# Kernel optimization log

Measured on AMD Instinct MI355X. Metric: run time of the kernel, lower is better.

## Reference

```python
import jax, jax.numpy as jnp
import numpy as np

FLOW_ITERS = 8
DUAL_ITERS = 8
DUAL_STEP = 0.1
DUAL_MOM = 0.9
GRAPH_LAYERS = 2
BIG = 1e9


def _sparsemax(z, mask):
    # sparsemax along last axis; masked entries already hold -BIG, zeroed by mask after.
    V = z.shape[-1]
    zs = jnp.sort(z, axis=-1)[..., ::-1]
    cum = jnp.cumsum(zs, axis=-1)
    k = jnp.arange(1, V + 1, dtype=z.dtype)
    support = zs * k > (cum - 1.0)
    k_sel = jnp.sum(support.astype(jnp.int32), axis=-1, keepdims=True)
    tau = (jnp.take_along_axis(cum, k_sel - 1, axis=-1) - 1.0) / k_sel.astype(z.dtype)
    return jnp.maximum(z - tau, 0.0) * mask


def _min_cost_flow(props, demands):
    # iterative proportional flow routing: push relu(inflow - demand) along predicted proportions
    def body(flow, _):
        inflow = jnp.sum(flow, axis=1)[..., None]      # [B,V,1] inflow to each node
        adjusted = jax.nn.relu(inflow - demands)       # excess to re-route
        return props * adjusted, None                  # row i scaled by its excess
    flow0 = jnp.zeros_like(props)
    flow, _ = jax.lax.scan(body, flow0, None, length=FLOW_ITERS)
    return flow


def _dual_flow(dual_diff, adj):
    # Nesterov-momentum projected gradient on cost(x)=x^2 minus linear dual term, x>=0 on edges
    def body(carry, _):
        flow, acc = carry
        look = flow - DUAL_MOM * acc
        grad = 2.0 * look - dual_diff                  # d/dx x^2 - dual_diff
        acc = DUAL_MOM * acc + DUAL_STEP * grad
        flow = adj * jax.nn.relu(flow - acc)
        return (flow, acc), None
    z = jnp.zeros_like(dual_diff)
    (flow, _), _ = jax.lax.scan(body, (z, z), None, length=DUAL_ITERS)
    return flow


def setup_inputs():
    key = jax.random.key(0)
    ks = jax.random.split(key, 32)
    B, V, F, E, D, K, H = 8, 1200, 8, 16, 64, 2, 4
    node_features = jax.random.normal(ks[0], (B, V, F), dtype=jnp.float32)
    node_embeddings = jax.random.normal(ks[1], (B, V, E), dtype=jnp.float32)
    d = jax.random.normal(ks[2], (B, V, 1), dtype=jnp.float32)
    demands = d - jnp.mean(d, axis=1, keepdims=True)   # balanced supply/demand per graph
    eye = jnp.eye(V, dtype=jnp.float32)
    adj = (jax.random.uniform(ks[3], (B, V, V)) < (16.0 / V)).astype(jnp.float32) * (1.0 - eye)
    hop2 = jnp.clip(adj @ adj, 0.0, 1.0) * (1.0 - eye)
    neighborhoods = jnp.stack([adj, hop2], axis=0)     # [K,B,V,V] k-hop neighborhoods

    def dense(k, fin, fout):
        return (jax.random.normal(k, (fin, fout), dtype=jnp.float32) / np.sqrt(fin)).astype(jnp.float32)

    return dict(
        node_features=node_features, node_embeddings=node_embeddings,
        demands=demands, adj=adj, neighborhoods=neighborhoods,
        enc_w0=dense(ks[4], E + F, D), enc_b0=jnp.zeros((D,), jnp.float32),
        enc_w1=dense(ks[5], D, D), enc_b1=jnp.zeros((D,), jnp.float32),
        agg_w=(jax.random.normal(ks[6], (K, D, D)) / np.sqrt(D)).astype(jnp.float32),
        agg_b=jnp.zeros((K, D), jnp.float32),
        att_w=(jax.random.normal(ks[7], (H, D, D)) / np.sqrt(D)).astype(jnp.float32),
        att_b=jnp.zeros((H, D), jnp.float32),
        att_v=(jax.random.normal(ks[8], (H, D)) / np.sqrt(D)).astype(jnp.float32),
        gru_wu=dense(ks[9], 2 * D, D), gru_bu=jnp.zeros((D,), jnp.float32),
        gru_wr=dense(ks[10], 2 * D, D), gru_br=jnp.zeros((D,), jnp.float32),
        gru_wc=dense(ks[11], 2 * D, D), gru_bc=jnp.zeros((D,), jnp.float32),
        dec_w0=dense(ks[12], D, D), dec_b0=jnp.zeros((D,), jnp.float32),
        dec_w1=dense(ks[13], D, 1), dec_b1=jnp.zeros((1,), jnp.float32),
        dual_w0=dense(ks[14], D, D), dual_b0=jnp.zeros((D,), jnp.float32),
        dual_w1=dense(ks[15], D, 1), dual_b1=jnp.zeros((1,), jnp.float32),
    )


def reference(node_features, node_embeddings, demands, adj, neighborhoods,
              enc_w0, enc_b0, enc_w1, enc_b1, agg_w, agg_b, att_w, att_b, att_v,
              gru_wu, gru_bu, gru_wr, gru_br, gru_wc, gru_bc,
              dec_w0, dec_b0, dec_w1, dec_b1, dual_w0, dual_b0, dual_w1, dual_b1):
    H = att_w.shape[0]
    # node encoder MLP (tanh hidden, tanh final since activate_final=True)
    x = jnp.concatenate([node_embeddings, node_features], axis=-1)
    enc = jnp.tanh(jnp.tanh(x @ enc_w0 + enc_b0) @ enc_w1 + enc_b1)            # [B,V,D]

    deg = jnp.sum(neighborhoods, axis=-1, keepdims=True)
    nb_norm = neighborhoods / jnp.maximum(deg, 1.0)                            # [K,B,V,V]

    for _ in range(GRAPH_LAYERS):
        # per-hop neighborhood aggregation
        msg = jnp.einsum('kbuv,bvd->kbud', nb_norm, enc)
        agg = jnp.tanh(jnp.einsum('kbud,kde->kbue', msg, agg_w) + agg_b[:, None, None, :])
        # multi-head attention over the K hop levels
        proj = jnp.tanh(jnp.einsum('kbvd,hde->hkbve', agg, att_w) + att_b[:, None, None, None, :])
        scores = jnp.einsum('hkbve,he->hkbv', proj, att_v)
        attn = jax.nn.softmax(scores, axis=1)                                  # softmax over hops
        nxt = jnp.einsum('hkbv,kbvd->bvd', attn, agg) / H                      # mean over heads
        # GRU state update
        xs = jnp.concatenate([nxt, enc], axis=-1)
        u = jax.nn.sigmoid(xs @ gru_wu + gru_bu)
        r = jax.nn.sigmoid(xs @ gru_wr + gru_br)
        c = jnp.tanh(jnp.concatenate([nxt, r * enc], axis=-1) @ gru_wc + gru_bc)
        enc = u * enc + (1.0 - u) * c

    # primal: edge weights -> sparsemax -> min-cost-flow
    pred = (enc @ dec_w0 + dec_b0) @ dec_w1 + dec_b1                           # [B,V,1]
    pred_weights = adj * jnp.transpose(pred, (0, 2, 1))                        # [B,V,V]
    weights = -BIG * (1.0 - adj) + pred_weights
    flow_props = _sparsemax(weights, adj)
    flow = _min_cost_flow(flow_props, demands)
    flow_cost = jnp.sum(flow * flow, axis=(1, 2))                              # square cost

    # dual: potentials -> dual-diff -> dual flow solver
    dual = (enc @ dual_w0 + dual_b0) @ dual_w1 + dual_b1                       # [B,V,1]
    dual_diff = adj * (dual - jnp.transpose(dual, (0, 2, 1)))
    dflow = _dual_flow(dual_diff, adj)
    dual_demand = jnp.sum(dual * demands, axis=(1, 2))
    dual_cost = jnp.sum(dflow * dflow - dual_diff * dflow, axis=(1, 2)) - dual_demand

    return flow_cost - dual_cost                                               # duality-gap loss, [B]
```

## Files before the change

### kernel.cpp

```cpp
#include <hip/hip_runtime.h>

#define BB 8
#define VV 1200
#define DD 64
#define KH 2
#define NH 4
#define CAP 64
#define NB2CAP 384
#define NROW (BB*VV)
#define NKROW (KH*BB*VV)

__device__ __forceinline__ float wredsum(float v) {
#pragma unroll
  for (int o = 32; o > 0; o >>= 1) v += __shfl_xor(v, o, 64);
  return v;
}
__device__ __forceinline__ float gredsum32(float v) {
#pragma unroll
  for (int o = 16; o > 0; o >>= 1) v += __shfl_xor(v, o, 64);
  return v;
}

__device__ __forceinline__ float tanh_f(float x) {
  float e = __expf(2.0f * x);
  return 1.0f - 2.0f / (e + 1.0f);
}
__device__ __forceinline__ float sigmoid_f(float x) { return 1.0f / (1.0f + __expf(-x)); }

__device__ __forceinline__ size_t nb_base(int row) {
  return (row < NROW) ? (size_t)row * CAP
                      : (size_t)NROW * CAP + (size_t)(row - NROW) * NB2CAP;
}

#define ENC2B (NROW / 64)
#define CSR2B (NKROW / 8)
__global__ void __launch_bounds__(512) k_pre(
    const float* __restrict__ nb, int* __restrict__ nb_cols, int* __restrict__ nb_cnt,
    const float* __restrict__ emb, const float* __restrict__ feat,
    const float* __restrict__ w0, const float* __restrict__ b0,
    const float* __restrict__ w1, const float* __restrict__ b1,
    float* __restrict__ enc0,
    int* __restrict__ col_cnt, float* __restrict__ out, int out_size) {
  __shared__ float Xe[64][25];
  __shared__ float Ht[64][65];
  __shared__ int colS[8][NB2CAP];
  int bid = blockIdx.x;
  int tid = threadIdx.x;
  if (bid < ENC2B) {
    int tile0 = bid * 64;
    if (tid < 256) {
      int i = tid >> 2, f = tid & 3;
      float4 e4 = *(const float4*)(emb + (size_t)(tile0 + i) * 16 + f * 4);
      Xe[i][f * 4] = e4.x; Xe[i][f * 4 + 1] = e4.y; Xe[i][f * 4 + 2] = e4.z; Xe[i][f * 4 + 3] = e4.w;
    } else if (tid < 384) {
      int t = tid - 256; int i = t >> 1, f = t & 1;
      float4 f4 = *(const float4*)(feat + (size_t)(tile0 + i) * 8 + f * 4);
      Xe[i][16 + f * 4] = f4.x; Xe[i][16 + f * 4 + 1] = f4.y;
      Xe[i][16 + f * 4 + 2] = f4.z; Xe[i][16 + f * 4 + 3] = f4.w;
    }
    __syncthreads();
    int rsub = tid >> 4, cg = tid & 15;
    int c0 = cg * 4, r0 = rsub * 2;
    float a[2][4];
#pragma unroll
    for (int i = 0; i < 2; ++i)
#pragma unroll
      for (int j = 0; j < 4; ++j) a[i][j] = b0[c0 + j];
#pragma unroll
    for (int kk = 0; kk < 24; ++kk) {
      float4 w4 = *(const float4*)(w0 + kk * DD + c0);
      float x0 = Xe[r0][kk], x1 = Xe[r0 + 1][kk];
      a[0][0] = fmaf(x0, w4.x, a[0][0]); a[0][1] = fmaf(x0, w4.y, a[0][1]);
      a[0][2] = fmaf(x0, w4.z, a[0][2]); a[0][3] = fmaf(x0, w4.w, a[0][3]);
      a[1][0] = fmaf(x1, w4.x, a[1][0]); a[1][1] = fmaf(x1, w4.y, a[1][1]);
      a[1][2] = fmaf(x1, w4.z, a[1][2]); a[1][3] = fmaf(x1, w4.w, a[1][3]);
    }
#pragma unroll
    for (int i = 0; i < 2; ++i) {
      Ht[r0 + i][c0] = tanh_f(a[i][0]); Ht[r0 + i][c0 + 1] = tanh_f(a[i][1]);
      Ht[r0 + i][c0 + 2] = tanh_f(a[i][2]); Ht[r0 + i][c0 + 3] = tanh_f(a[i][3]);
    }
    __syncthreads();
    float g[2][4];
#pragma unroll
    for (int i = 0; i < 2; ++i)
#pragma unroll
      for (int j = 0; j < 4; ++j) g[i][j] = b1[c0 + j];
#pragma unroll 8
    for (int kk = 0; kk < DD; ++kk) {
      float4 w4 = *(const float4*)(w1 + kk * DD + c0);
      float x0 = Ht[r0][kk], x1 = Ht[r0 + 1][kk];
      g[0][0] = fmaf(x0, w4.x, g[0][0]); g[0][1] = fmaf(x0, w4.y, g[0][1]);
      g[0][2] = fmaf(x0, w4.z, g[0][2]); g[0][3] = fmaf(x0, w4.w, g[0][3]);
      g[1][0] = fmaf(x1, w4.x, g[1][0]); g[1][1] = fmaf(x1, w4.y, g[1][1]);
      g[1][2] = fmaf(x1, w4.z, g[1][2]); g[1][3] = fmaf(x1, w4.w, g[1][3]);
    }
#pragma unroll
    for (int i = 0; i < 2; ++i) {
      float4 o;
      o.x = tanh_f(g[i][0]); o.y = tanh_f(g[i][1]);
      o.z = tanh_f(g[i][2]); o.w = tanh_f(g[i][3]);
      *(float4*)(enc0 + (size_t)(tile0 + r0 + i) * DD + c0) = o;
    }
  } else if (bid < ENC2B + CSR2B) {
    int w = tid >> 6, lane = tid & 63;
    int row = (bid - ENC2B) * 8 + w;
    const float4* nb4 = (const float4*)(nb + (size_t)row * VV);
    float4 v[5];
#pragma unroll
    for (int c = 0; c < 4; ++c) v[c] = nb4[c * 64 + lane];
    v[4].x = v[4].y = v[4].z = v[4].w = 0.0f;
    if (lane < 44) v[4] = nb4[256 + lane];
    unsigned long long ltmask = (lane == 0) ? 0ull : ((1ull << lane) - 1ull);
    size_t base = nb_base(row);
    int cap = (row < NROW) ? CAP : NB2CAP;
    int off_base = 0;
#pragma unroll
    for (int c = 0; c < 5; ++c) {
      int nz0 = (v[c].x != 0.0f), nz1 = (v[c].y != 0.0f);
      int nz2 = (v[c].z != 0.0f), nz3 = (v[c].w != 0.0f);
      unsigned long long m0 = __ballot(nz0 != 0);
      unsigned long long m1 = __ballot(nz1 != 0);
      unsigned long long m2 = __ballot(nz2 != 0);
      unsigned long long m3 = __ballot(nz3 != 0);
      int lanepref = __popcll(m0 & ltmask) + __popcll(m1 & ltmask)
                   + __popcll(m2 & ltmask) + __popcll(m3 & ltmask);
      int chunkcnt = __popcll(m0) + __popcll(m1) + __popcll(m2) + __popcll(m3);
      int off = off_base + lanepref;
      int vi = (c * 64 + lane) * 4;
      if (nz0 && off < cap) colS[w][off] = vi;
      off += nz0;
      if (nz1 && off < cap) colS[w][off] = vi + 1;
      off += nz1;
      if (nz2 && off < cap) colS[w][off] = vi + 2;
      off += nz2;
      if (nz3 && off < cap) colS[w][off] = vi + 3;
      off_base += chunkcnt;
    }
    int ncp = (off_base > cap) ? cap : off_base;
    if (lane == 0) nb_cnt[row] = ncp;
    for (int j = lane; j < ncp; j += 64) nb_cols[base + j] = colS[w][j];
  } else {
    for (int i = tid; i < NROW; i += 512) col_cnt[i] = 0;
    if (tid < out_size) out[tid] = 0.0f;
  }
}

__global__ void __launch_bounds__(256) k_gather(
    const int* __restrict__ nb_cols, const int* __restrict__ nb_cnt,
    const float* __restrict__ encIn, float* __restrict__ msg) {
  int w = threadIdx.x >> 6, lane = threadIdx.x & 63;
  int row = blockIdx.x * 4 + w;
  int k = (row >= NROW) ? 1 : 0;
  int bv = row - k * NROW;
  int b = bv / VV;
  const float4* encF = (const float4*)(encIn + (size_t)b * VV * DD);
  const int* cols = nb_cols + nb_base(row);
  int n = nb_cnt[row];
  int sub = lane >> 4, q = lane & 15;
  float ax = 0.0f, ay = 0.0f, az = 0.0f, aw = 0.0f;
  int j = 0;
  int cc0 = 0, cc1 = 0, cc2 = 0, cc3 = 0;
  if (j + 16 <= n) {
    cc0 = cols[j + sub]; cc1 = cols[j + 4 + sub];
    cc2 = cols[j + 8 + sub]; cc3 = cols[j + 12 + sub];
  }
  while (j + 16 <= n) {
    int nj = j + 16;
    int p0 = 0, p1 = 0, p2 = 0, p3 = 0;
    if (nj + 16 <= n) {
      p0 = cols[nj + sub]; p1 = cols[nj + 4 + sub];
      p2 = cols[nj + 8 + sub]; p3 = cols[nj + 12 + sub];
    }
    float4 u0 = encF[(size_t)cc0 * 16 + q];
    float4 u1 = encF[(size_t)cc1 * 16 + q];
    float4 u2 = encF[(size_t)cc2 * 16 + q];
    float4 u3 = encF[(size_t)cc3 * 16 + q];
    ax += (u0.x + u1.x) + (u2.x + u3.x);
    ay += (u0.y + u1.y) + (u2.y + u3.y);
    az += (u0.z + u1.z) + (u2.z + u3.z);
    aw += (u0.w + u1.w) + (u2.w + u3.w);
    cc0 = p0; cc1 = p1; cc2 = p2; cc3 = p3;
    j = nj;
  }
  for (; j < n; j += 4) {
    int idx = j + sub;
    if (idx < n) {
      float4 u = encF[(size_t)cols[idx] * 16 + q];
      ax += u.x; ay += u.y; az += u.z; aw += u.w;
    }
  }
#pragma unroll
  for (int o = 16; o < 64; o <<= 1) {
    ax += __shfl_xor(ax, o, 64);
    ay += __shfl_xor(ay, o, 64);
    az += __shfl_xor(az, o, 64);
    aw += __shfl_xor(aw, o, 64);
  }
  if (lane < 16) {
    float inv = 1.0f / fmaxf((float)n, 1.0f);
    float4 r; r.x = ax * inv; r.y = ay * inv; r.z = az * inv; r.w = aw * inv;
    ((float4*)(msg + (size_t)row * DD))[q] = r;
  }
}

__global__ void __launch_bounds__(256) k_layer(
    const float* __restrict__ msg, const float* __restrict__ encIn,
    const float* __restrict__ agg_w, const float* __restrict__ agg_b,
    const float* __restrict__ att_w, const float* __restrict__ att_b,
    const float* __restrict__ att_v,
    const float* __restrict__ wu, const float* __restrict__ bu,
    const float* __restrict__ wr, const float* __restrict__ br,
    const float* __restrict__ wc, const float* __restrict__ bc,
    float* __restrict__ encOut,
    int do_decode,
    const float* __restrict__ dw0, const float* __restrict__ db0,
    const float* __restrict__ dw1, const float* __restrict__ db1,
    const float* __restrict__ uw0, const float* __restrict__ ub0,
    const float* __restrict__ uw1, const float* __restrict__ ub1,
    float* __restrict__ pred, float* __restrict__ dualp) {
  __shared__ float M[32][65];
  __shared__ float G[32][65];
  __shared__ float X[16][129];
  __shared__ float EO[16][65];
  __shared__ float scS[NH][KH][16];
  int tid = threadIdx.x;
  int t0 = blockIdx.x * 16;
#pragma unroll
  for (int rep = 0; rep < 2; ++rep) {
    int idx = rep * 256 + tid; int i = idx >> 4, d4 = idx & 15;
    int grow = (i < 16) ? (t0 + i) : (NROW + t0 + (i - 16));
    float4 m4 = *(const float4*)(msg + (size_t)grow * DD + d4 * 4);
    M[i][d4 * 4] = m4.x; M[i][d4 * 4 + 1] = m4.y; M[i][d4 * 4 + 2] = m4.z; M[i][d4 * 4 + 3] = m4.w;
  }
  __syncthreads();
  int strip = tid >> 5, cg2 = tid & 31;
  int c0 = cg2 * 2;
  int r0 = strip * 4;
  int k = strip >> 2;
  const float* W = agg_w + (size_t)k * DD * DD;
  float acc[4][2];
#pragma unroll
  for (int i = 0; i < 4; ++i) {
    acc[i][0] = agg_b[k * DD + c0]; acc[i][1] = agg_b[k * DD + c0 + 1];
  }
#pragma unroll 8
  for (int kk = 0; kk < DD; ++kk) {
    float2 w2 = *(const float2*)(W + kk * DD + c0);
#pragma unroll
    for (int i = 0; i < 4; ++i) {
      float x = M[r0 + i][kk];
      acc[i][0] = fmaf(x, w2.x, acc[i][0]); acc[i][1] = fmaf(x, w2.y, acc[i][1]);
    }
  }
#pragma unroll
  for (int i = 0; i < 4; ++i) {
    G[r0 + i][c0] = tanh_f(acc[i][0]);
    G[r0 + i][c0 + 1] = tanh_f(acc[i][1]);
  }
  __syncthreads();
#pragma unroll
  for (int h = 0; h < NH; ++h) {
    const float* Wh = att_w + (size_t)h * DD * DD;
    float a2[4][2];
#pragma unroll
    for (int i = 0; i < 4; ++i) {
      a2[i][0] = att_b[h * DD + c0]; a2[i][1] = att_b[h * DD + c0 + 1];
    }
#pragma unroll 8
    for (int kk = 0; kk < DD; ++kk) {
      float2 w2 = *(const float2*)(Wh + kk * DD + c0);
#pragma unroll
      for (int i = 0; i < 4; ++i) {
        float x = G[r0 + i][kk];
        a2[i][0] = fmaf(x, w2.x, a2[i][0]); a2[i][1] = fmaf(x, w2.y, a2[i][1]);
      }
    }
    float2 v2 = *(const float2*)(att_v + h * DD + c0);
#pragma unroll
    for (int i = 0; i < 4; ++i) {
      float p = tanh_f(a2[i][0]) * v2.x + tanh_f(a2[i][1]) * v2.y;
      p = gredsum32(p);
      if (cg2 == 0) scS[h][k][(strip & 3) * 4 + i] = p;
    }
  }
  __syncthreads();
  {
    int i = tid >> 4, d4 = tid & 15;
    float W0 = 0.0f, W1 = 0.0f;
#pragma unroll
    for (int h = 0; h < NH; ++h) {
      float s0 = scS[h][0][i];
      float s1 = scS[h][1][i];
      float m = fmaxf(s0, s1);
      float e0 = __expf(s0 - m), e1 = __expf(s1 - m);
      float inv = 1.0f / (e0 + e1);
      W0 += e0 * inv; W1 += e1 * inv;
    }
    W0 *= 0.25f; W1 *= 0.25f;
    float4 ef = *(const float4*)(encIn + (size_t)(t0 + i) * DD + d4 * 4);
#pragma unroll
    for (int j = 0; j < 4; ++j) {
      int d = d4 * 4 + j;
      X[i][d] = W0 * G[i][d] + W1 * G[16 + i][d];
    }
    X[i][64 + d4 * 4]     = ef.x;
    X[i][64 + d4 * 4 + 1] = ef.y;
    X[i][64 + d4 * 4 + 2] = ef.z;
    X[i][64 + d4 * 4 + 3] = ef.w;
  }
  __syncthreads();
  int gr0 = strip * 2;
  float au[2][2], ar[2][2];
#pragma unroll
  for (int i = 0; i < 2; ++i) {
    au[i][0] = bu[c0]; au[i][1] = bu[c0 + 1];
    ar[i][0] = br[c0]; ar[i][1] = br[c0 + 1];
  }
#pragma unroll 8
  for (int kk = 0; kk < 2 * DD; ++kk) {
    float2 u2 = *(const float2*)(wu + kk * DD + c0);
    float2 r2 = *(const float2*)(wr + kk * DD + c0);
#pragma unroll
    for (int i = 0; i < 2; ++i) {
      float x = X[gr0 + i][kk];
      au[i][0] = fmaf(x, u2.x, au[i][0]); au[i][1] = fmaf(x, u2.y, au[i][1]);
      ar[i][0] = fmaf(x, r2.x, ar[i][0]); ar[i][1] = fmaf(x, r2.y, ar[i][1]);
    }
  }
  float uu[2][2], encv[2][2];
#pragma unroll
  for (int i = 0; i < 2; ++i) {
    uu[i][0] = sigmoid_f(au[i][0]); uu[i][1] = sigmoid_f(au[i][1]);
    encv[i][0] = X[gr0 + i][64 + c0]; encv[i][1] = X[gr0 + i][64 + c0 + 1];
  }
  __syncthreads();
#pragma unroll
  for (int i = 0; i < 2; ++i) {
    X[gr0 + i][64 + c0]     = encv[i][0] * sigmoid_f(ar[i][0]);
    X[gr0 + i][64 + c0 + 1] = encv[i][1] * sigmoid_f(ar[i][1]);
  }
  __syncthreads();
  float ac[2][2];
#pragma unroll
  for (int i = 0; i < 2; ++i) { ac[i][0] = bc[c0]; ac[i][1] = bc[c0 + 1]; }
#pragma unroll 8
  for (int kk = 0; kk < 2 * DD; ++kk) {
    float2 c2 = *(const float2*)(wc + kk * DD + c0);
#pragma unroll
    for (int i = 0; i < 2; ++i) {
      float x = X[gr0 + i][kk];
      ac[i][0] = fmaf(x, c2.x, ac[i][0]); ac[i][1] = fmaf(x, c2.y, ac[i][1]);
    }
  }
#pragma unroll
  for (int i = 0; i < 2; ++i) {
    float e0 = uu[i][0] * encv[i][0] + (1.0f - uu[i][0]) * tanh_f(ac[i][0]);
    float e1 = uu[i][1] * encv[i][1] + (1.0f - uu[i][1]) * tanh_f(ac[i][1]);
    *(float2*)(encOut + (size_t)(t0 + gr0 + i) * DD + c0) = make_float2(e0, e1);
    EO[gr0 + i][c0] = e0; EO[gr0 + i][c0 + 1] = e1;
  }
  if (do_decode) {
    __syncthreads();
    float hd[2][2], hq[2][2];
#pragma unroll
    for (int i = 0; i < 2; ++i) {
      hd[i][0] = db0[c0]; hd[i][1] = db0[c0 + 1];
      hq[i][0] = ub0[c0]; hq[i][1] = ub0[c0 + 1];
    }
#pragma unroll 8
    for (int kk = 0; kk < DD; ++kk) {
      float2 d2 = *(const float2*)(dw0 + kk * DD + c0);
      float2 q2 = *(const float2*)(uw0 + kk * DD + c0);
#pragma unroll
      for (int i = 0; i < 2; ++i) {
        float x = EO[gr0 + i][kk];
        hd[i][0] = fmaf(x, d2.x, hd[i][0]); hd[i][1] = fmaf(x, d2.y, hd[i][1]);
        hq[i][0] = fmaf(x, q2.x, hq[i][0]); hq[i][1] = fmaf(x, q2.y, hq[i][1]);
      }
    }
    float2 dv = *(const float2*)(dw1 + c0);
    float2 qv = *(const float2*)(uw1 + c0);
#pragma unroll
    for (int i = 0; i < 2; ++i) {
      float p = hd[i][0] * dv.x + hd[i][1] * dv.y;
      float q = hq[i][0] * qv.x + hq[i][1] * qv.y;
      p = gredsum32(p);
      q = gredsum32(q);
      if (cg2 == 0) {
        pred[t0 + gr0 + i] = p + db1[0];
        dualp[t0 + gr0 + i] = q + ub1[0];
      }
    }
  }
}

__global__ void __launch_bounds__(256) k_primal_dual(
    const int* __restrict__ nb_cols, const int* __restrict__ nb_cnt,
    const float* __restrict__ pred, const float* __restrict__ dualp,
    const float* __restrict__ dem,
    float* __restrict__ rowsum,
    int* __restrict__ col_cnt, int* __restrict__ col_rows, float* __restrict__ col_vals,
    float* __restrict__ out) {
  __shared__ float bacc[BB];
  if (threadIdx.x < BB) bacc[threadIdx.x] = 0.0f;
  __syncthreads();
  int w = threadIdx.x >> 6, lane = threadIdx.x & 63;
  int row = blockIdx.x * 4 + w;
  int b = row / VV;
  int n = nb_cnt[row];
  int c = (lane < n) ? nb_cols[(size_t)row * CAP + lane] : 0;
  const float* predB = pred + (size_t)b * VV;
  const float* dualB = dualp + (size_t)b * VV;
  float z = (lane < n) ? predB[c] : -1e30f;
  float tau = 0.0f;
  if (n > 0) {
    bool in = (lane < n);
    for (int it = 0; it < 64; ++it) {
      float s = wredsum(in ? z : 0.0f);
      int cnt = (int)__popcll(__ballot(in));
      tau = (s - 1.0f) / (float)cnt;
      bool nin = (z > tau);
      if (__ballot(nin) == __ballot(in)) break;
      in = nin;
    }
  }
  float pv = (lane < n) ? fmaxf(z - tau, 0.0f) : 0.0f;
  float s2 = wredsum(pv * pv);
  if (lane == 0) rowsum[row] = s2;
  if (pv > 0.0f) {
    int g = b * VV + c;
    int j = atomicAdd(&col_cnt[g], 1);
    if (j < CAP) {
      col_rows[(size_t)g * CAP + j] = row - b * VV;
      col_vals[(size_t)g * CAP + j] = pv;
    }
  }
  float du = dualp[row];
  float es = 0.0f;
  if (lane < n) {
    float dd = du - dualB[c];
    float f = 0.0f, acm = 0.0f;
#pragma unroll
    for (int t = 0; t < 8; ++t) {
      float look = f - 0.9f * acm;
      float grad = 2.0f * look - dd;
      acm = 0.9f * acm + 0.1f * grad;
      f = fmaxf(f - acm, 0.0f);
    }
    es = f * f - dd * f;
  }
  float contrib = -es;
  if (lane == 0) contrib += du * dem[row];
  float ws_ = wredsum(contrib);
  if (lane == 0) atomicAdd(&bacc[b], ws_);
  __syncthreads();
  if (threadIdx.x < BB) {
    float t = bacc[threadIdx.x];
    if (t != 0.0f) atomicAdd(&out[threadIdx.x], t);
  }
}

__global__ void __launch_bounds__(1024) k_flow(
    const int* __restrict__ col_cnt, const int* __restrict__ col_rows,
    const float* __restrict__ col_vals, const float* __restrict__ dem,
    const float* __restrict__ rowsum, float* __restrict__ out) {
  __shared__ float aS[VV];
  __shared__ float red[16];
  int b = blockIdx.x;
  int tid = threadIdx.x;
  const float* demB = dem + (size_t)b * VV;
  for (int v = tid; v < VV; v += 1024) aS[v] = fmaxf(-demB[v], 0.0f);
  __syncthreads();
  for (int t = 0; t < 7; ++t) {
    float nv0 = 0.0f, nv1 = 0.0f;
    {
      int v = tid;
      if (v < VV) {
        int g = b * VV + v;
        int n = col_cnt[g]; if (n > CAP) n = CAP;
        const int* cr = col_rows + (size_t)g * CAP;
        const float* cv = col_vals + (size_t)g * CAP;
        float acc = 0.0f;
        for (int j = 0; j < n; ++j) acc += cv[j] * aS[cr[j]];
        nv0 = fmaxf(acc - demB[v], 0.0f);
      }
      v = tid + 1024;
      if (v < VV) {
        int g = b * VV + v;
        int n = col_cnt[g]; if (n > CAP) n = CAP;
        const int* cr = col_rows + (size_t)g * CAP;
        const float* cv = col_vals + (size_t)g * CAP;
        float acc = 0.0f;
        for (int j = 0; j < n; ++j) acc += cv[j] * aS[cr[j]];
        nv1 = fmaxf(acc - demB[v], 0.0f);
      }
    }
    __syncthreads();
    if (tid < VV) aS[tid] = nv0;
    if (tid + 1024 < VV) aS[tid + 1024] = nv1;
    __syncthreads();
  }
  float fc = 0.0f;
  for (int v = tid; v < VV; v += 1024) { float a = aS[v]; fc += a * a * rowsum[b * VV + v]; }
  fc = wredsum(fc);
  int wid = tid >> 6, lane = tid & 63;
  if (lane == 0) red[wid] = fc;
  __syncthreads();
  if (tid == 0) {
    float s = 0.0f;
#pragma unroll
    for (int i = 0; i < 16; ++i) s += red[i];
    atomicAdd(&out[b], s);
  }
}

extern "C" void kernel_launch(void* const* d_in, const int* in_sizes, int n_in,
                              void* d_out, int out_size, void* d_ws, size_t ws_size,
                              hipStream_t stream) {
  const float* feat   = (const float*)d_in[0];
  const float* emb    = (const float*)d_in[1];
  const float* dem    = (const float*)d_in[2];
  const float* nb     = (const float*)d_in[4];
  const float* enc_w0 = (const float*)d_in[5];
  const float* enc_b0 = (const float*)d_in[6];
  const float* enc_w1 = (const float*)d_in[7];
  const float* enc_b1 = (const float*)d_in[8];
  const float* agg_w  = (const float*)d_in[9];
  const float* agg_b  = (const float*)d_in[10];
  const float* att_w  = (const float*)d_in[11];
  const float* att_b  = (const float*)d_in[12];
  const float* att_v  = (const float*)d_in[13];
  const float* gru_wu = (const float*)d_in[14];
  const float* gru_bu = (const float*)d_in[15];
  const float* gru_wr = (const float*)d_in[16];
  const float* gru_br = (const float*)d_in[17];
  const float* gru_wc = (const float*)d_in[18];
  const float* gru_bc = (const float*)d_in[19];
  const float* dec_w0 = (const float*)d_in[20];
  const float* dec_b0 = (const float*)d_in[21];
  const float* dec_w1 = (const float*)d_in[22];
  const float* dec_b1 = (const float*)d_in[23];
  const float* dual_w0= (const float*)d_in[24];
  const float* dual_b0= (const float*)d_in[25];
  const float* dual_w1= (const float*)d_in[26];
  const float* dual_b1= (const float*)d_in[27];
  float* out = (float*)d_out;

  float* enc0 = (float*)d_ws;
  float* enc1 = enc0 + (size_t)NROW * DD;
  float* msg      = enc1 + (size_t)NROW * DD;
  float* pred     = msg + (size_t)NKROW * DD;
  float* dualp    = pred + NROW;
  float* rowsum   = dualp + NROW;
  float* col_vals = rowsum + NROW;
  int* col_cnt  = (int*)(col_vals + (size_t)NROW * CAP);
  int* nb_cnt   = col_cnt + NROW;
  int* col_rows = nb_cnt + NKROW;
  int* nb_cols  = col_rows + (size_t)NROW * CAP;

  (void)in_sizes; (void)n_in; (void)ws_size;

  k_pre<<<ENC2B + CSR2B + 1, 512, 0, stream>>>(
      nb, nb_cols, nb_cnt, emb, feat, enc_w0, enc_b0, enc_w1, enc_b1, enc0,
      col_cnt, out, out_size);

  const float* encIn = enc0;
  float* encOut = enc1;
  for (int l = 0; l < 2; ++l) {
    k_gather<<<NKROW / 4, 256, 0, stream>>>(nb_cols, nb_cnt, encIn, msg);
    k_layer<<<NROW / 16, 256, 0, stream>>>(msg, encIn,
                                           agg_w, agg_b, att_w, att_b, att_v,
                                           gru_wu, gru_bu, gru_wr, gru_br, gru_wc, gru_bc,
                                           encOut,
                                           (l == 1) ? 1 : 0,
                                           dec_w0, dec_b0, dec_w1, dec_b1,
                                           dual_w0, dual_b0, dual_w1, dual_b1, pred, dualp);
    const float* t = encIn; encIn = encOut; encOut = (float*)t;
  }

  k_primal_dual<<<NROW / 4, 256, 0, stream>>>(nb_cols, nb_cnt, pred, dualp, dem,
                                              rowsum, col_cnt, col_rows, col_vals, out);
  k_flow<<<BB, 1024, 0, stream>>>(col_cnt, col_rows, col_vals, dem, rowsum, out);
}
```

Before: 514.4 us.

## Stage layer weight matrices through shared memory instead of global loads

The k_layer kernel now cooperatively copies each weight matrix (agg, attention in two halves, GRU u/r/c, decoder) into a 32KB shared buffer before the matching matmul, and reads weights from LDS instead of global/L2 per-thread float2 loads. To fit, M and G are merged into one buffer, and the fused u/r GEMV is split into two passes. This trades repeated global weight traffic per block for extra syncthreads, large staging copies per block (600 blocks each reloading all weights), and higher LDS use that may cut occupancy.

```diff
diff --git a/kernel.cpp b/kernel.cpp
--- a/kernel.cpp
+++ b/kernel.cpp
@@ -219,26 +219,31 @@
     const float* __restrict__ uw0, const float* __restrict__ ub0,
     const float* __restrict__ uw1, const float* __restrict__ ub1,
     float* __restrict__ pred, float* __restrict__ dualp) {
-  __shared__ float M[32][65];
-  __shared__ float G[32][65];
+  __shared__ float MG[32][65];
   __shared__ float X[16][129];
   __shared__ float EO[16][65];
   __shared__ float scS[NH][KH][16];
+  __shared__ float WS[8192];
   int tid = threadIdx.x;
   int t0 = blockIdx.x * 16;
+#pragma unroll
+  for (int p = 0; p < 8; ++p) {
+    int idx = p * 256 + tid;
+    ((float4*)WS)[idx] = ((const float4*)agg_w)[idx];
+  }
 #pragma unroll
   for (int rep = 0; rep < 2; ++rep) {
     int idx = rep * 256 + tid; int i = idx >> 4, d4 = idx & 15;
     int grow = (i < 16) ? (t0 + i) : (NROW + t0 + (i - 16));
     float4 m4 = *(const float4*)(msg + (size_t)grow * DD + d4 * 4);
-    M[i][d4 * 4] = m4.x; M[i][d4 * 4 + 1] = m4.y; M[i][d4 * 4 + 2] = m4.z; M[i][d4 * 4 + 3] = m4.w;
+    MG[i][d4 * 4] = m4.x; MG[i][d4 * 4 + 1] = m4.y;
+    MG[i][d4 * 4 + 2] = m4.z; MG[i][d4 * 4 + 3] = m4.w;
   }
   __syncthreads();
   int strip = tid >> 5, cg2 = tid & 31;
   int c0 = cg2 * 2;
   int r0 = strip * 4;
   int k = strip >> 2;
-  const float* W = agg_w + (size_t)k * DD * DD;
   float acc[4][2];
 #pragma unroll
   for (int i = 0; i < 4; ++i) {
@@ -246,22 +251,27 @@
   }
 #pragma unroll 8
   for (int kk = 0; kk < DD; ++kk) {
-    float2 w2 = *(const float2*)(W + kk * DD + c0);
+    float2 w2 = *(const float2*)(&WS[k * 4096 + kk * DD + c0]);
 #pragma unroll
     for (int i = 0; i < 4; ++i) {
-      float x = M[r0 + i][kk];
+      float x = MG[r0 + i][kk];
       acc[i][0] = fmaf(x, w2.x, acc[i][0]); acc[i][1] = fmaf(x, w2.y, acc[i][1]);
     }
   }
+  __syncthreads();
 #pragma unroll
   for (int i = 0; i < 4; ++i) {
-    G[r0 + i][c0] = tanh_f(acc[i][0]);
-    G[r0 + i][c0 + 1] = tanh_f(acc[i][1]);
-  }
-  __syncthreads();
-#pragma unroll
-  for (int h = 0; h < NH; ++h) {
-    const float* Wh = att_w + (size_t)h * DD * DD;
+    MG[r0 + i][c0] = tanh_f(acc[i][0]);
+    MG[r0 + i][c0 + 1] = tanh_f(acc[i][1]);
+  }
+#pragma unroll
+  for (int p = 0; p < 8; ++p) {
+    int idx = p * 256 + tid;
+    ((float4*)WS)[idx] = ((const float4*)att_w)[idx];
+  }
+  __syncthreads();
+#pragma unroll
+  for (int h = 0; h < 2; ++h) {
     float a2[4][2];
 #pragma unroll
     for (int i = 0; i < 4; ++i) {
@@ -269,10 +279,10 @@
     }
 #pragma unroll 8
     for (int kk = 0; kk < DD; ++kk) {
-      float2 w2 = *(const float2*)(Wh + kk * DD + c0);
+      float2 w2 = *(const float2*)(&WS[h * 4096 + kk * DD + c0]);
 #pragma unroll
       for (int i = 0; i < 4; ++i) {
-        float x = G[r0 + i][kk];
+        float x = MG[r0 + i][kk];
         a2[i][0] = fmaf(x, w2.x, a2[i][0]); a2[i][1] = fmaf(x, w2.y, a2[i][1]);
       }
     }
@@ -285,6 +295,43 @@
     }
   }
   __syncthreads();
+#pragma unroll
+  for (int p = 0; p < 8; ++p) {
+    int idx = p * 256 + tid;
+    ((float4*)WS)[idx] = ((const float4*)(att_w + 2 * 4096))[idx];
+  }
+  __syncthreads();
+#pragma unroll
+  for (int h = 0; h < 2; ++h) {
+    int hh = 2 + h;
+    float a2[4][2];
+#pragma unroll
+    for (int i = 0; i < 4; ++i) {
+      a2[i][0] = att_b[hh * DD + c0]; a2[i][1] = att_b[hh * DD + c0 + 1];
+    }
+#pragma unroll 8
+    for (int kk = 0; kk < DD; ++kk) {
+      float2 w2 = *(const float2*)(&WS[h * 4096 + kk * DD + c0]);
+#pragma unroll
+      for (int i = 0; i < 4; ++i) {
+        float x = MG[r0 + i][kk];
+        a2[i][0] = fmaf(x, w2.x, a2[i][0]); a2[i][1] = fmaf(x, w2.y, a2[i][1]);
+      }
+    }
+    float2 v2 = *(const float2*)(att_v + hh * DD + c0);
+#pragma unroll
+    for (int i = 0; i < 4; ++i) {
+      float p = tanh_f(a2[i][0]) * v2.x + tanh_f(a2[i][1]) * v2.y;
+      p = gredsum32(p);
+      if (cg2 == 0) scS[hh][k][(strip & 3) * 4 + i] = p;
+    }
+  }
+  __syncthreads();
+#pragma unroll
+  for (int p = 0; p < 8; ++p) {
+    int idx = p * 256 + tid;
+    ((float4*)WS)[idx] = ((const float4*)wu)[idx];
+  }
   {
     int i = tid >> 4, d4 = tid & 15;
     float W0 = 0.0f, W1 = 0.0f;
@@ -302,7 +349,7 @@
 #pragma unroll
     for (int j = 0; j < 4; ++j) {
       int d = d4 * 4 + j;
-      X[i][d] = W0 * G[i][d] + W1 * G[16 + i][d];
+      X[i][d] = W0 * MG[i][d] + W1 * MG[16 + i][d];
     }
     X[i][64 + d4 * 4]     = ef.x;
     X[i][64 + d4 * 4 + 1] = ef.y;
@@ -311,21 +358,16 @@
   }
   __syncthreads();
   int gr0 = strip * 2;
-  float au[2][2], ar[2][2];
-#pragma unroll
-  for (int i = 0; i < 2; ++i) {
-    au[i][0] = bu[c0]; au[i][1] = bu[c0 + 1];
-    ar[i][0] = br[c0]; ar[i][1] = br[c0 + 1];
-  }
+  float au[2][2];
+#pragma unroll
+  for (int i = 0; i < 2; ++i) { au[i][0] = bu[c0]; au[i][1] = bu[c0 + 1]; }
 #pragma unroll 8
   for (int kk = 0; kk < 2 * DD; ++kk) {
-    float2 u2 = *(const float2*)(wu + kk * DD + c0);
-    float2 r2 = *(const float2*)(wr + kk * DD + c0);
+    float2 u2 = *(const float2*)(&WS[kk * DD + c0]);
 #pragma unroll
     for (int i = 0; i < 2; ++i) {
       float x = X[gr0 + i][kk];
       au[i][0] = fmaf(x, u2.x, au[i][0]); au[i][1] = fmaf(x, u2.y, au[i][1]);
-      ar[i][0] = fmaf(x, r2.x, ar[i][0]); ar[i][1] = fmaf(x, r2.y, ar[i][1]);
     }
   }
   float uu[2][2], encv[2][2];
@@ -336,17 +378,41 @@
   }
   __syncthreads();
 #pragma unroll
+  for (int p = 0; p < 8; ++p) {
+    int idx = p * 256 + tid;
+    ((float4*)WS)[idx] = ((const float4*)wr)[idx];
+  }
+  __syncthreads();
+  float ar[2][2];
+#pragma unroll
+  for (int i = 0; i < 2; ++i) { ar[i][0] = br[c0]; ar[i][1] = br[c0 + 1]; }
+#pragma unroll 8
+  for (int kk = 0; kk < 2 * DD; ++kk) {
+    float2 r2 = *(const float2*)(&WS[kk * DD + c0]);
+#pragma unroll
+    for (int i = 0; i < 2; ++i) {
+      float x = X[gr0 + i][kk];
+      ar[i][0] = fmaf(x, r2.x, ar[i][0]); ar[i][1] = fmaf(x, r2.y, ar[i][1]);
+    }
+  }
+  __syncthreads();
+#pragma unroll
   for (int i = 0; i < 2; ++i) {
     X[gr0 + i][64 + c0]     = encv[i][0] * sigmoid_f(ar[i][0]);
     X[gr0 + i][64 + c0 + 1] = encv[i][1] * sigmoid_f(ar[i][1]);
   }
+#pragma unroll
+  for (int p = 0; p < 8; ++p) {
+    int idx = p * 256 + tid;
+    ((float4*)WS)[idx] = ((const float4*)wc)[idx];
+  }
   __syncthreads();
   float ac[2][2];
 #pragma unroll
   for (int i = 0; i < 2; ++i) { ac[i][0] = bc[c0]; ac[i][1] = bc[c0 + 1]; }
 #pragma unroll 8
   for (int kk = 0; kk < 2 * DD; ++kk) {
-    float2 c2 = *(const float2*)(wc + kk * DD + c0);
+    float2 c2 = *(const float2*)(&WS[kk * DD + c0]);
 #pragma unroll
     for (int i = 0; i < 2; ++i) {
       float x = X[gr0 + i][kk];
@@ -362,6 +428,13 @@
   }
   if (do_decode) {
     __syncthreads();
+#pragma unroll
+    for (int p = 0; p < 4; ++p) {
+      int idx = p * 256 + tid;
+      ((float4*)WS)[idx] = ((const float4*)dw0)[idx];
+      ((float4*)WS)[1024 + idx] = ((const float4*)uw0)[idx];
+    }
+    __syncthreads();
     float hd[2][2], hq[2][2];
 #pragma unroll
     for (int i = 0; i < 2; ++i) {
@@ -370,8 +443,8 @@
     }
 #pragma unroll 8
     for (int kk = 0; kk < DD; ++kk) {
-      float2 d2 = *(const float2*)(dw0 + kk * DD + c0);
-      float2 q2 = *(const float2*)(uw0 + kk * DD + c0);
+      float2 d2 = *(const float2*)(&WS[kk * DD + c0]);
+      float2 q2 = *(const float2*)(&WS[4096 + kk * DD + c0]);
 #pragma unroll
       for (int i = 0; i < 2; ++i) {
         float x = EO[gr0 + i][kk];
```

Result: faster. 486.5 us (-5.4%).
